# Kernel optimization log

Hardware: AMD Instinct MI355X
Metric: run time of the kernel (lower is better)

## Reference

```python
import jax, jax.numpy as jnp
import numpy as np

DIM = 384
WIN = 64
HEADS = 12
B_ = 4096


def setup_inputs() -> dict:
    key = jax.random.key(0)
    k1, k2, k3, k4, k5 = jax.random.split(key, 5)
    x = jax.random.normal(k1, (B_, WIN, DIM), dtype=jnp.float32)
    # torch Linear weights: qkv.weight [3*dim, dim], proj.weight [dim, dim], proj.bias [dim]
    qkv_w = jax.random.normal(k2, (3 * DIM, DIM), dtype=jnp.float32) * (DIM ** -0.5)
    proj_w = jax.random.normal(k3, (DIM, DIM), dtype=jnp.float32) * (DIM ** -0.5)
    proj_b = jax.random.normal(k4, (DIM,), dtype=jnp.float32) * 0.02
    bias_table = jax.random.normal(k5, (2 * WIN - 1, HEADS), dtype=jnp.float32) * 0.02
    return {"x": x, "qkv_w": qkv_w, "proj_w": proj_w, "proj_b": proj_b,
            "bias_table": bias_table}


def reference(x, qkv_w, proj_w, proj_b, bias_table):
    B, N, C = x.shape
    H = HEADS
    hd = C // H
    scale = hd ** -0.5
    # qkv projection (torch: x @ W.T), split into q,k,v [B,H,N,hd]
    qkv = jnp.einsum('bnc,dc->bnd', x, qkv_w)
    qkv = qkv.reshape(B, N, 3, H, hd).transpose(2, 0, 3, 1, 4)
    q, k, v = qkv[0] * scale, qkv[1], qkv[2]
    attn = jnp.einsum('bhnd,bhmd->bhnm', q, k)  # [B,H,N,N]
    # relative position bias: index [N,N] into table [2W-1,H]
    coords = jnp.arange(N)
    rel_idx = coords[:, None] - coords[None, :] + (N - 1)  # [N,N]
    bias = bias_table[rel_idx]  # [N,N,H]
    attn = attn + bias.transpose(2, 0, 1)[None]
    attn = jax.nn.softmax(attn, axis=-1)
    out = jnp.einsum('bhnm,bhmd->bhnd', attn, v)
    out = out.transpose(0, 2, 1, 3).reshape(B, N, C)
    out = jnp.einsum('bnc,dc->bnd', out, proj_w) + proj_b
    return out
```

## Files before the change

kernel.cpp:

```cpp
#include <hip/hip_runtime.h>
#include <stdint.h>

#define DIM 384
#define WIN 64
#define HEADS 12
#define HD 32
#define NWIN 4096

typedef _Float16 f16;
typedef unsigned int u32;
typedef _Float16 half8 __attribute__((ext_vector_type(8)));
typedef _Float16 half4 __attribute__((ext_vector_type(4)));
typedef float floatx4 __attribute__((ext_vector_type(4)));

#define AS1 __attribute__((address_space(1)))
#define AS3 __attribute__((address_space(3)))

__device__ __forceinline__ void gl_lds16(const void* g, void* l) {
    __builtin_amdgcn_global_load_lds((const AS1 u32*)g, (AS3 u32*)l, 16, 0, 0);
}

__global__ void cvt_kernel(const float* __restrict__ in, f16* __restrict__ out, long n4) {
    long i = (long)blockIdx.x * blockDim.x + threadIdx.x;
    const long stride = (long)gridDim.x * blockDim.x;
    for (; i < n4; i += stride) {
        float4 v = ((const float4*)in)[i];
        half4 h;
        h[0] = (f16)v.x; h[1] = (f16)v.y; h[2] = (f16)v.z; h[3] = (f16)v.w;
        ((half4*)out)[i] = h;
    }
}

__global__ void qkv_kernel(const float* __restrict__ A32, const f16* __restrict__ Bw,
                           f16* __restrict__ q_arr, f16* __restrict__ k_arr,
                           f16* __restrict__ v_int, int nwg)
{
    __shared__ __align__(16) f16 xa[2][128][32];

    int lin = blockIdx.x;
    int nlin = lin;
    if ((nwg & 7) == 0) nlin = (lin & 7) * (nwg >> 3) + (lin >> 3);
    const int colb = nlin % 9, rowb = nlin / 9;
    const int col0 = colb * 128, row0 = rowb * 128;

    const int tid = threadIdx.x;
    const int wave = tid >> 6, lane = tid & 63;
    const int g = lane >> 4, c = lane & 15;
    const int wm = wave >> 1, wn = wave & 1;

    floatx4 acc[4][4] = {};
    float4 rA[4];

    auto loadA = [&](int t) {
        const int k0 = t * 32;
#pragma unroll
        for (int r = 0; r < 4; ++r) {
            const int i = r * 256 + tid;
            const int row = i >> 3, kq = i & 7;
            rA[r] = *(const float4*)(A32 + (size_t)(row0 + row) * DIM + k0 + kq * 4);
        }
    };
    auto writeA = [&](int nb) {
#pragma unroll
        for (int r = 0; r < 4; ++r) {
            const int i = r * 256 + tid;
            const int row = i >> 3, kq = i & 7;
            const int sl = (kq >> 1) ^ ((row >> 1) & 3);
            half4 h;
            h[0] = (f16)rA[r].x; h[1] = (f16)rA[r].y;
            h[2] = (f16)rA[r].z; h[3] = (f16)rA[r].w;
            *(half4*)&xa[nb][row][sl * 8 + (kq & 1) * 4] = h;
        }
    };

    loadA(0);
    writeA(0);

#pragma unroll 2
    for (int s = 0; s < 12; ++s) {
        __syncthreads();
        if (s < 11) loadA(s + 1);

        half8 bf[4];
#pragma unroll
        for (int i = 0; i < 4; ++i)
            bf[i] = *(const half8*)(Bw + (size_t)(col0 + wn * 64 + i * 16 + c) * DIM
                                    + s * 32 + g * 8);
        half8 af[4];
#pragma unroll
        for (int i = 0; i < 4; ++i) {
            const int row = wm * 64 + i * 16 + c;
            const int sl = g ^ ((row >> 1) & 3);
            af[i] = *(const half8*)&xa[s & 1][row][sl * 8];
        }
#pragma unroll
        for (int mi = 0; mi < 4; ++mi)
#pragma unroll
            for (int ni = 0; ni < 4; ++ni)
                acc[mi][ni] = __builtin_amdgcn_mfma_f32_16x16x32_f16(
                    af[mi], bf[ni], acc[mi][ni], 0, 0, 0);
        if (s < 11) writeA((s + 1) & 1);
    }

    const int which = colb / 3;
    const int dbase = col0 - which * DIM;
    const int b0 = rowb * 2 + wm;
    if (which < 2) {
        f16* dst = which ? k_arr : q_arr;
        const float sc = which ? 1.0f : 0.17677669529663687f;
#pragma unroll
        for (int ni = 0; ni < 4; ++ni) {
            const int d = dbase + wn * 64 + ni * 16 + c;
            const int h = d >> 5, e = d & 31;
            f16* base = dst + (size_t)(b0 * HEADS + h) * (WIN * HD) + e;
#pragma unroll
            for (int mi = 0; mi < 4; ++mi)
#pragma unroll
                for (int j = 0; j < 4; ++j) {
                    const int n = mi * 16 + g * 4 + j;
                    base[(size_t)n * HD] = (f16)(acc[mi][ni][j] * sc);
                }
        }
    } else {
#pragma unroll
        for (int ni = 0; ni < 4; ++ni) {
            const int d = dbase + wn * 64 + ni * 16 + c;
            const int h = d >> 5, e = d & 31;
            f16* vb = v_int + (size_t)(b0 * HEADS + h) * (WIN * HD);
#pragma unroll
            for (int mi = 0; mi < 4; ++mi) {
                const int n0 = mi * 16 + g * 4;
                half4 pk;
#pragma unroll
                for (int j = 0; j < 4; ++j) pk[j] = (f16)acc[mi][ni][j];
                *(half4*)(vb + (n0 >> 3) * 256 + e * 8 + (n0 & 7)) = pk;
            }
        }
    }
}

__global__ void proj_kernel(const f16* __restrict__ A, const f16* __restrict__ Bw,
                            float* __restrict__ outp, const float* __restrict__ proj_b,
                            int nwg)
{
    __shared__ __align__(16) f16 lds[3][2][4][128][8];

    int lin = blockIdx.x;
    int nlin = lin;
    if ((nwg & 7) == 0) nlin = (lin & 7) * (nwg >> 3) + (lin >> 3);
    const int colb = nlin % 3, rowb = nlin / 3;
    const int col0 = colb * 128, row0 = rowb * 128;

    const int tid = threadIdx.x;
    const int wave = tid >> 6, lane = tid & 63;
    const int g = lane >> 4, c = lane & 15;
    const int wm = wave >> 1, wn = wave & 1;

    floatx4 acc[4][4] = {};

    auto stage = [&](int t) {
        const int k0 = t * 32;
#pragma unroll
        for (int r = 0; r < 4; ++r) {
            const int u = wave + r * 4;
            const int isB = u >> 3;
            const int uu = u & 7;
            const int kc = uu >> 1, m0 = (uu & 1) * 64;
            const f16* src = (isB ? Bw + (size_t)(col0 + m0 + lane) * DIM
                                  : A  + (size_t)(row0 + m0 + lane) * DIM)
                             + k0 + kc * 8;
            gl_lds16(src, &lds[t % 3][isB][kc][m0][0]);
        }
    };

    stage(0); stage(1);

#pragma unroll
    for (int s = 0; s < 12; ++s) {
        if (s < 11) asm volatile("s_waitcnt vmcnt(4)" ::: "memory");
        else        asm volatile("s_waitcnt vmcnt(0)" ::: "memory");
        asm volatile("s_waitcnt lgkmcnt(0)" ::: "memory");
        __builtin_amdgcn_sched_barrier(0);
        __builtin_amdgcn_s_barrier();
        __builtin_amdgcn_sched_barrier(0);
        if (s < 10) stage(s + 2);

        half8 af[4], bf[4];
#pragma unroll
        for (int i = 0; i < 4; ++i) {
            af[i] = *(const half8*)&lds[s % 3][0][g][wm * 64 + i * 16 + c][0];
            bf[i] = *(const half8*)&lds[s % 3][1][g][wn * 64 + i * 16 + c][0];
        }
#pragma unroll
        for (int mi = 0; mi < 4; ++mi)
#pragma unroll
            for (int ni = 0; ni < 4; ++ni)
                acc[mi][ni] = __builtin_amdgcn_mfma_f32_16x16x32_f16(
                    af[mi], bf[ni], acc[mi][ni], 0, 0, 0);
    }

#pragma unroll
    for (int ni = 0; ni < 4; ++ni) {
        const int d = col0 + wn * 64 + ni * 16 + c;
        const float pb = proj_b[d];
#pragma unroll
        for (int mi = 0; mi < 4; ++mi)
#pragma unroll
            for (int j = 0; j < 4; ++j) {
                const size_t trow = (size_t)row0 + wm * 64 + mi * 16 + g * 4 + j;
                outp[trow * DIM + d] = acc[mi][ni][j] + pb;
            }
    }
}

__global__ void attn_kernel(const f16* __restrict__ q_arr, const f16* __restrict__ k_arr,
                            const f16* __restrict__ v_int,
                            const float* __restrict__ bias_table,
                            f16* __restrict__ attn_out)
{
    const int bid = blockIdx.x;
    const int bw = bid / HEADS, h = bid % HEADS;
    const f16* q = q_arr + (size_t)bid * (WIN * HD);
    const f16* k = k_arr + (size_t)bid * (WIN * HD);
    const f16* v = v_int + (size_t)bid * (WIN * HD);

    const int tid = threadIdx.x;
    const int w = tid >> 6, lane = tid & 63;
    const int g = lane >> 4, c = lane & 15;

    __shared__ float bias_lds[2 * WIN - 1];
    __shared__ __align__(16) f16 p_lds[8][64][8];

    for (int i = tid; i < 2 * WIN - 1; i += 256)
        bias_lds[i] = bias_table[(size_t)i * HEADS + h];
    __syncthreads();

    half8 qa = *(const half8*)(q + (16 * w + c) * HD + g * 8);
    floatx4 s[4];
#pragma unroll
    for (int t = 0; t < 4; ++t) {
        half8 kb = *(const half8*)(k + (16 * t + c) * HD + g * 8);
        floatx4 z = {};
        s[t] = __builtin_amdgcn_mfma_f32_16x16x32_f16(qa, kb, z, 0, 0, 0);
    }

    float pr[4][4];
#pragma unroll
    for (int j = 0; j < 4; ++j) {
        const int n = 16 * w + g * 4 + j;
        float mx = -1e30f;
#pragma unroll
        for (int t = 0; t < 4; ++t) {
            const int m = 16 * t + c;
            pr[j][t] = s[t][j] + bias_lds[n - m + 63];
            mx = fmaxf(mx, pr[j][t]);
        }
        mx = fmaxf(mx, __shfl_xor(mx, 1));
        mx = fmaxf(mx, __shfl_xor(mx, 2));
        mx = fmaxf(mx, __shfl_xor(mx, 4));
        mx = fmaxf(mx, __shfl_xor(mx, 8));
        float sum = 0.f;
#pragma unroll
        for (int t = 0; t < 4; ++t) { pr[j][t] = __expf(pr[j][t] - mx); sum += pr[j][t]; }
        sum += __shfl_xor(sum, 1);
        sum += __shfl_xor(sum, 2);
        sum += __shfl_xor(sum, 4);
        sum += __shfl_xor(sum, 8);
        const float r = 1.0f / sum;
#pragma unroll
        for (int t = 0; t < 4; ++t) {
            const int m = 16 * t + c;
            p_lds[m >> 3][n][m & 7] = (f16)(pr[j][t] * r);
        }
    }
    __syncthreads();

    half8 pa0 = *(const half8*)&p_lds[g][16 * w + c][0];
    half8 pa1 = *(const half8*)&p_lds[4 + g][16 * w + c][0];
    floatx4 o[2];
#pragma unroll
    for (int t = 0; t < 2; ++t) {
        half8 vb0 = *(const half8*)(v + g * 256 + (16 * t + c) * 8);
        half8 vb1 = *(const half8*)(v + (4 + g) * 256 + (16 * t + c) * 8);
        floatx4 z = {};
        o[t] = __builtin_amdgcn_mfma_f32_16x16x32_f16(pa0, vb0, z, 0, 0, 0);
        o[t] = __builtin_amdgcn_mfma_f32_16x16x32_f16(pa1, vb1, o[t], 0, 0, 0);
    }
#pragma unroll
    for (int t = 0; t < 2; ++t)
#pragma unroll
        for (int j = 0; j < 4; ++j) {
            const int n = 16 * w + g * 4 + j;
            attn_out[((size_t)bw * WIN + n) * DIM + h * HD + 16 * t + c] = (f16)o[t][j];
        }
}

extern "C" void kernel_launch(void* const* d_in, const int* in_sizes, int n_in,
                              void* d_out, int out_size, void* d_ws, size_t ws_size,
                              hipStream_t stream) {
    const float* x          = (const float*)d_in[0];
    const float* qkv_w      = (const float*)d_in[1];
    const float* proj_w     = (const float*)d_in[2];
    const float* proj_b     = (const float*)d_in[3];
    const float* bias_table = (const float*)d_in[4];
    float* out = (float*)d_out;
    (void)in_sizes; (void)n_in; (void)out_size;

    uintptr_t p = (uintptr_t)d_ws;
    auto carve = [&](size_t bytes) -> void* {
        uintptr_t q = p; p += (bytes + 255) & ~(size_t)255; return (void*)q;
    };
    f16* w16_qkv  = (f16*)carve((size_t)3 * DIM * DIM * 2);
    f16* w16_proj = (f16*)carve((size_t)DIM * DIM * 2);
    const size_t fixed = p - (uintptr_t)d_ws;

    int CB = NWIN;
    while (CB > 16 && fixed + (size_t)CB * 196608 + 4096 > ws_size) CB >>= 1;

    f16* qa = (f16*)carve((size_t)CB * HEADS * WIN * HD * 2);
    f16* ka = (f16*)carve((size_t)CB * HEADS * WIN * HD * 2);
    f16* vi = (f16*)carve((size_t)CB * HEADS * WIN * HD * 2);
    f16* ao = (f16*)carve((size_t)CB * WIN * DIM * 2);

    cvt_kernel<<<dim3(256), dim3(256), 0, stream>>>(qkv_w, w16_qkv, (long)(3 * DIM * DIM / 4));
    cvt_kernel<<<dim3(64),  dim3(256), 0, stream>>>(proj_w, w16_proj, (long)(DIM * DIM / 4));

    for (int c0 = 0; c0 < NWIN; c0 += CB) {
        const float* xc = x + (size_t)c0 * WIN * DIM;

        const int nwg1 = (CB * WIN / 128) * 9;
        qkv_kernel<<<dim3(nwg1), dim3(256), 0, stream>>>(xc, w16_qkv, qa, ka, vi, nwg1);

        attn_kernel<<<dim3(CB * HEADS), dim3(256), 0, stream>>>(qa, ka, vi, bias_table, ao);

        const int nwg2 = (CB * WIN / 128) * 3;
        proj_kernel<<<dim3(nwg2), dim3(256), 0, stream>>>(ao, w16_proj,
                                                          out + (size_t)c0 * WIN * DIM, proj_b, nwg2);
    }
}
```

Baseline: 1.034 ms.

## Pre-pack x and QKV weights into tiles and stream via global_load_lds triple buffer

Adds a separate pass that converts x to f16 in a tile-major layout, and packs the QKV weights the same way. The QKV GEMM can then stage both operands straight into LDS with async global_load_lds, using a three-deep ring buffer and fewer barriers per step. This removes the per-block fp32 load and convert work, and the uncached direct global reads of B fragments. In exchange it writes and reads back an extra f16 copy of x (more HBM traffic, one more launch) and needs more LDS per block, which may lower occupancy.

```diff
diff --git a/kernel.cpp b/kernel.cpp
--- a/kernel.cpp
+++ b/kernel.cpp
@@ -31,17 +31,52 @@
     }
 }
 
-__global__ void qkv_kernel(const float* __restrict__ A32, const f16* __restrict__ Bw,
+__global__ void pack_w_kernel(const float* __restrict__ w, f16* __restrict__ Bp) {
+    const int t = blockIdx.x * 256 + threadIdx.x;
+    const int colb = t / 6144;
+    const int r1 = t % 6144;
+    const int s = r1 / 512;
+    const int r2 = r1 % 512;
+    const int kc = r2 >> 7, u = r2 & 127;
+    const float* sp = w + (size_t)(colb * 128 + u) * DIM + s * 32 + kc * 8;
+    float4 a = *(const float4*)sp;
+    float4 b = *(const float4*)(sp + 4);
+    half8 o;
+    o[0] = (f16)a.x; o[1] = (f16)a.y; o[2] = (f16)a.z; o[3] = (f16)a.w;
+    o[4] = (f16)b.x; o[5] = (f16)b.y; o[6] = (f16)b.z; o[7] = (f16)b.w;
+    *(half8*)(Bp + (size_t)t * 8) = o;
+}
+
+__global__ void pack_x_kernel(const float* __restrict__ x, f16* __restrict__ Xp) {
+    const int b = blockIdx.x;
+    const int s = b % 12;
+    const int rowb = b / 12;
+    const int t = threadIdx.x;
+    const int kc = t & 3, rr = t >> 2;
+#pragma unroll
+    for (int h = 0; h < 2; ++h) {
+        const int row = rr + h * 64;
+        const float* sp = x + (size_t)(rowb * 128 + row) * DIM + s * 32 + kc * 8;
+        float4 a = *(const float4*)sp;
+        float4 bq = *(const float4*)(sp + 4);
+        half8 o;
+        o[0] = (f16)a.x;  o[1] = (f16)a.y;  o[2] = (f16)a.z;  o[3] = (f16)a.w;
+        o[4] = (f16)bq.x; o[5] = (f16)bq.y; o[6] = (f16)bq.z; o[7] = (f16)bq.w;
+        *(half8*)(Xp + ((size_t)b * 512 + kc * 128 + row) * 8) = o;
+    }
+}
+
+__global__ void qkv_kernel(const f16* __restrict__ Xp, const f16* __restrict__ Bp,
                            f16* __restrict__ q_arr, f16* __restrict__ k_arr,
                            f16* __restrict__ v_int, int nwg)
 {
-    __shared__ __align__(16) f16 xa[2][128][32];
+    __shared__ __align__(16) f16 ldsA[3][4096];
+    __shared__ __align__(16) f16 ldsB[3][4096];
 
     int lin = blockIdx.x;
     int nlin = lin;
     if ((nwg & 7) == 0) nlin = (lin & 7) * (nwg >> 3) + (lin >> 3);
     const int colb = nlin % 9, rowb = nlin / 9;
-    const int col0 = colb * 128, row0 = rowb * 128;
 
     const int tid = threadIdx.x;
     const int wave = tid >> 6, lane = tid & 63;
@@ -49,49 +84,36 @@
     const int wm = wave >> 1, wn = wave & 1;
 
     floatx4 acc[4][4] = {};
-    float4 rA[4];
-
-    auto loadA = [&](int t) {
-        const int k0 = t * 32;
-#pragma unroll
-        for (int r = 0; r < 4; ++r) {
-            const int i = r * 256 + tid;
-            const int row = i >> 3, kq = i & 7;
-            rA[r] = *(const float4*)(A32 + (size_t)(row0 + row) * DIM + k0 + kq * 4);
+
+    auto stage = [&](int t) {
+        const f16* sa = Xp + (size_t)(rowb * 12 + t) * 4096;
+        const f16* sb = Bp + (size_t)(colb * 12 + t) * 4096;
+        f16* da = &ldsA[t % 3][0];
+        f16* db = &ldsB[t % 3][0];
+#pragma unroll
+        for (int r = 0; r < 2; ++r) {
+            const int ch = r * 256 + tid;
+            gl_lds16(sa + (size_t)ch * 8, da + (size_t)ch * 8);
+            gl_lds16(sb + (size_t)ch * 8, db + (size_t)ch * 8);
         }
     };
-    auto writeA = [&](int nb) {
-#pragma unroll
-        for (int r = 0; r < 4; ++r) {
-            const int i = r * 256 + tid;
-            const int row = i >> 3, kq = i & 7;
-            const int sl = (kq >> 1) ^ ((row >> 1) & 3);
-            half4 h;
-            h[0] = (f16)rA[r].x; h[1] = (f16)rA[r].y;
-            h[2] = (f16)rA[r].z; h[3] = (f16)rA[r].w;
-            *(half4*)&xa[nb][row][sl * 8 + (kq & 1) * 4] = h;
-        }
-    };
-
-    loadA(0);
-    writeA(0);
-
-#pragma unroll 2
+
+    stage(0); stage(1);
+
+#pragma unroll
     for (int s = 0; s < 12; ++s) {
-        __syncthreads();
-        if (s < 11) loadA(s + 1);
-
-        half8 bf[4];
-#pragma unroll
-        for (int i = 0; i < 4; ++i)
-            bf[i] = *(const half8*)(Bw + (size_t)(col0 + wn * 64 + i * 16 + c) * DIM
-                                    + s * 32 + g * 8);
-        half8 af[4];
+        if (s < 11) asm volatile("s_waitcnt vmcnt(4)" ::: "memory");
+        else        asm volatile("s_waitcnt vmcnt(0)" ::: "memory");
+        __builtin_amdgcn_sched_barrier(0);
+        __builtin_amdgcn_s_barrier();
+        __builtin_amdgcn_sched_barrier(0);
+        if (s < 10) stage(s + 2);
+
+        half8 af[4], bf[4];
 #pragma unroll
         for (int i = 0; i < 4; ++i) {
-            const int row = wm * 64 + i * 16 + c;
-            const int sl = g ^ ((row >> 1) & 3);
-            af[i] = *(const half8*)&xa[s & 1][row][sl * 8];
+            af[i] = *(const half8*)&ldsA[s % 3][g * 1024 + (wm * 64 + i * 16 + c) * 8];
+            bf[i] = *(const half8*)&ldsB[s % 3][g * 1024 + (wn * 64 + i * 16 + c) * 8];
         }
 #pragma unroll
         for (int mi = 0; mi < 4; ++mi)
@@ -99,9 +121,9 @@
             for (int ni = 0; ni < 4; ++ni)
                 acc[mi][ni] = __builtin_amdgcn_mfma_f32_16x16x32_f16(
                     af[mi], bf[ni], acc[mi][ni], 0, 0, 0);
-        if (s < 11) writeA((s + 1) & 1);
-    }
-
+    }
+
+    const int col0 = colb * 128;
     const int which = colb / 3;
     const int dbase = col0 - which * DIM;
     const int b0 = rowb * 2 + wm;
@@ -310,30 +332,34 @@
     auto carve = [&](size_t bytes) -> void* {
         uintptr_t q = p; p += (bytes + 255) & ~(size_t)255; return (void*)q;
     };
-    f16* w16_qkv  = (f16*)carve((size_t)3 * DIM * DIM * 2);
     f16* w16_proj = (f16*)carve((size_t)DIM * DIM * 2);
+    f16* Bp       = (f16*)carve((size_t)9 * 12 * 512 * 8 * 2);
     const size_t fixed = p - (uintptr_t)d_ws;
 
     int CB = NWIN;
-    while (CB > 16 && fixed + (size_t)CB * 196608 + 4096 > ws_size) CB >>= 1;
-
+    while (CB > 16 && fixed + (size_t)CB * 245760 + 4096 > ws_size) CB >>= 1;
+
+    f16* Xp = (f16*)carve((size_t)CB * WIN * DIM * 2);
     f16* qa = (f16*)carve((size_t)CB * HEADS * WIN * HD * 2);
     f16* ka = (f16*)carve((size_t)CB * HEADS * WIN * HD * 2);
     f16* vi = (f16*)carve((size_t)CB * HEADS * WIN * HD * 2);
     f16* ao = (f16*)carve((size_t)CB * WIN * DIM * 2);
 
-    cvt_kernel<<<dim3(256), dim3(256), 0, stream>>>(qkv_w, w16_qkv, (long)(3 * DIM * DIM / 4));
-    cvt_kernel<<<dim3(64),  dim3(256), 0, stream>>>(proj_w, w16_proj, (long)(DIM * DIM / 4));
+    cvt_kernel<<<dim3(64), dim3(256), 0, stream>>>(proj_w, w16_proj, (long)(DIM * DIM / 4));
+    pack_w_kernel<<<dim3(216), dim3(256), 0, stream>>>(qkv_w, Bp);
 
     for (int c0 = 0; c0 < NWIN; c0 += CB) {
         const float* xc = x + (size_t)c0 * WIN * DIM;
-
-        const int nwg1 = (CB * WIN / 128) * 9;
-        qkv_kernel<<<dim3(nwg1), dim3(256), 0, stream>>>(xc, w16_qkv, qa, ka, vi, nwg1);
+        const int rowbs = CB / 2;
+
+        pack_x_kernel<<<dim3(rowbs * 12), dim3(256), 0, stream>>>(xc, Xp);
+
+        const int nwg1 = rowbs * 9;
+        qkv_kernel<<<dim3(nwg1), dim3(256), 0, stream>>>(Xp, Bp, qa, ka, vi, nwg1);
 
         attn_kernel<<<dim3(CB * HEADS), dim3(256), 0, stream>>>(qa, ka, vi, bias_table, ao);
 
-        const int nwg2 = (CB * WIN / 128) * 3;
+        const int nwg2 = rowbs * 3;
         proj_kernel<<<dim3(nwg2), dim3(256), 0, stream>>>(ao, w16_proj,
                                                           out + (size_t)c0 * WIN * DIM, proj_b, nwg2);
     }
```

Measured after the change: 917.8 us. 11.2% less time.
